# Kernel tuning notes

Hardware: AMD Instinct MI355X
Metric: run time of the kernel (lower is better)

Reference implementation:

```python
import jax, jax.numpy as jnp
import numpy as np

NEG_INF = -1e30


def _cc_attention(q, k, v):
    # q,k: [B,H,W,c], v: [B,H,W,C]
    B, H, W, _ = q.shape
    # vertical scores over column: [B,H,W,H], diag (h==g) masked out
    sv = jnp.einsum('bhwc,bgwc->bhwg', q, k)
    eye = jnp.eye(H, dtype=bool)[:, None, :]  # [H,1,H]
    sv = jnp.where(eye, NEG_INF, sv)
    # horizontal scores over row: [B,H,W,W]
    sh = jnp.einsum('bhwc,bhuc->bhwu', q, k)
    a = jax.nn.softmax(jnp.concatenate([sv, sh], axis=-1), axis=-1)
    av, ah = a[..., :H], a[..., H:H + W]
    yv = jnp.einsum('bhwg,bgwc->bhwc', av, v)
    yh = jnp.einsum('bhwu,bhuc->bhwc', ah, v)
    return yv + yh


def setup_inputs() -> dict:
    key = jax.random.key(0)
    ks = jax.random.split(key, 7)
    B, H, W, C = 8, 96, 96, 512
    c = C // 8
    s = lambda n: 1.0 / np.sqrt(n)
    return {
        'x': jax.random.normal(ks[0], (B, H, W, C), jnp.float32),
        'Wq': jax.random.normal(ks[1], (C, c), jnp.float32) * s(C),
        'bq': jnp.zeros((c,), jnp.float32),
        'Wk': jax.random.normal(ks[2], (C, c), jnp.float32) * s(C),
        'bk': jnp.zeros((c,), jnp.float32),
        'Wv': jax.random.normal(ks[3], (C, C), jnp.float32) * s(C),
        'bv': jnp.zeros((C,), jnp.float32),
        'gamma': jnp.float32(0.5),
    }


def reference(x, Wq, bq, Wk, bk, Wv, bv, gamma):
    # 1x1 convs == per-pixel matmul
    q = jnp.einsum('bhwc,cd->bhwd', x, Wq) + bq
    k = jnp.einsum('bhwc,cd->bhwd', x, Wk) + bk
    v = jnp.einsum('bhwc,cd->bhwd', x, Wv) + bv
    y = _cc_attention(q, k, v) * gamma
    return y + x
```

## Files before the change

kernel.cpp:

```cpp
#include <hip/hip_runtime.h>
#include <hip/hip_bf16.h>


#define NPIX 73728
#define HH 96
#define WW 96
#define CC 512
#define CQ 64
#define PA 384

typedef __attribute__((ext_vector_type(8))) short bf16x8;
typedef __attribute__((ext_vector_type(4))) float f32x4;

__device__ __forceinline__ void async16(const void* g, void* l) {
    __builtin_amdgcn_global_load_lds(
        (const __attribute__((address_space(1))) unsigned int*)g,
        (__attribute__((address_space(3))) unsigned int*)l,
        16, 0, 0);
}

__device__ __forceinline__ short bf16s(float f) {
    __hip_bfloat16 h = __float2bfloat16(f);
    return *reinterpret_cast<short*>(&h);
}

__global__ __launch_bounds__(256) void conv_x(
    const float* __restrict__ x, short* __restrict__ xb)
{
    size_t i8 = ((size_t)blockIdx.x * 256 + threadIdx.x) * 8;
    float4 a = *reinterpret_cast<const float4*>(x + i8);
    float4 b = *reinterpret_cast<const float4*>(x + i8 + 4);
    union { __hip_bfloat16 h[8]; uint4 u; } pk;
    pk.h[0] = __float2bfloat16(a.x); pk.h[1] = __float2bfloat16(a.y);
    pk.h[2] = __float2bfloat16(a.z); pk.h[3] = __float2bfloat16(a.w);
    pk.h[4] = __float2bfloat16(b.x); pk.h[5] = __float2bfloat16(b.y);
    pk.h[6] = __float2bfloat16(b.z); pk.h[7] = __float2bfloat16(b.w);
    *reinterpret_cast<uint4*>(xb + i8) = pk.u;
}

__global__ __launch_bounds__(256) void conv_w(
    const float* __restrict__ W, short* __restrict__ dst, int J)
{
    int idx = blockIdx.x * 256 + threadIdx.x;
    int lane = idx & 63;
    int blk = idx >> 6;
    int ntiles = J >> 4;
    int ntile = blk % ntiles;
    int kb32 = blk / ntiles;
    int krow = kb32 * 32 + (lane >> 4) * 8;
    int col = ntile * 16 + (lane & 15);
    union { __hip_bfloat16 h[8]; uint4 u; } pk;
    #pragma unroll
    for (int j = 0; j < 8; ++j)
        pk.h[j] = __float2bfloat16(W[(size_t)(krow + j) * J + col]);
    *reinterpret_cast<uint4*>(dst + (size_t)idx * 8) = pk.u;
}

template <int BN>
__global__ __launch_bounds__(256) void mfma_proj(
    const short* __restrict__ Xb,
    const short* __restrict__ Wf,
    const float* __restrict__ bias,
    short* __restrict__ out,
    int J)
{
    __shared__ __align__(16) short Albuf[128 * 32];
    const int tid = threadIdx.x;
    const int lane = tid & 63;
    const int w = tid >> 6;
    const int mBase = blockIdx.x * 128;
    const int nBase = blockIdx.y * BN;

    constexpr int MT = (BN == 128) ? 4 : 2;
    constexpr int NT = 4;
    const int wr = (BN == 128) ? (w >> 1) : w;
    const int wc = (BN == 128) ? (w & 1) : 0;
    const int tbase = wr * MT;
    const int nTile0 = (nBase >> 4) + wc * 4;
    const int ntilesJ = J >> 4;

    f32x4 acc[MT][NT];
    #pragma unroll
    for (int i = 0; i < MT; ++i)
        #pragma unroll
        for (int j = 0; j < NT; ++j) {
            f32x4 z = {0.f, 0.f, 0.f, 0.f};
            acc[i][j] = z;
        }

    const int arow0 = lane & 15;
    const int acol0 = (lane >> 4) * 8;

    for (int kb = 0; kb < 16; ++kb) {
        #pragma unroll
        for (int s = 0; s < 2; ++s) {
            int t = w * 2 + s;
            const short* g = Xb + (size_t)(mBase + t * 16 + arow0) * 512 + kb * 32 + acol0;
            async16(g, &Albuf[t * 512]);
        }
        __syncthreads();

        bf16x8 bf[NT];
        #pragma unroll
        for (int jn = 0; jn < NT; ++jn)
            bf[jn] = *reinterpret_cast<const bf16x8*>(
                Wf + ((size_t)(kb * ntilesJ + nTile0 + jn) * 64 + lane) * 8);
        bf16x8 af[MT];
        #pragma unroll
        for (int i = 0; i < MT; ++i)
            af[i] = *reinterpret_cast<const bf16x8*>(&Albuf[(tbase + i) * 512 + lane * 8]);
        #pragma unroll
        for (int i = 0; i < MT; ++i)
            #pragma unroll
            for (int jn = 0; jn < NT; ++jn)
                acc[i][jn] = __builtin_amdgcn_mfma_f32_16x16x32_bf16(
                    af[i], bf[jn], acc[i][jn], 0, 0, 0);
        __syncthreads();
    }

    const int lrow = (lane >> 4) * 4, lcol = lane & 15;
    #pragma unroll
    for (int jn = 0; jn < NT; ++jn) {
        int col = nBase + wc * 64 + jn * 16 + lcol;
        float bc = bias[col];
        #pragma unroll
        for (int i = 0; i < MT; ++i) {
            int row = mBase + wr * (MT * 16) + i * 16 + lrow;
            #pragma unroll
            for (int r = 0; r < 4; ++r) {
                out[(size_t)(row + r) * J + col] = bf16s(acc[i][jn][r] + bc);
            }
        }
    }
}

__global__ __launch_bounds__(256) void proj_v_th(
    const short* __restrict__ Xb,
    const short* __restrict__ Wf,
    const float* __restrict__ bias,
    short* __restrict__ vth)
{
    __shared__ __align__(16) short Albuf[128 * 32];
    const int tid = threadIdx.x;
    const int lane = tid & 63;
    const int w = tid >> 6;
    const int bid = blockIdx.x;
    const int mBase = (bid >> 2) * 128;
    const int nBase = (bid & 3) * 128;

    const int wr = w >> 1, wc = w & 1;
    const int nTile0 = (nBase >> 4) + wc * 4;

    f32x4 acc[4][4];
    #pragma unroll
    for (int i = 0; i < 4; ++i)
        #pragma unroll
        for (int j = 0; j < 4; ++j) {
            f32x4 z = {0.f, 0.f, 0.f, 0.f};
            acc[i][j] = z;
        }

    const int arow0 = lane & 15;
    const int acol0 = (lane >> 4) * 8;

    for (int kb = 0; kb < 16; ++kb) {
        #pragma unroll
        for (int s = 0; s < 2; ++s) {
            int t = w * 2 + s;
            const short* g = Xb + (size_t)(mBase + t * 16 + arow0) * 512 + kb * 32 + acol0;
            async16(g, &Albuf[t * 512]);
        }
        __syncthreads();

        bf16x8 bf[4];
        #pragma unroll
        for (int jn = 0; jn < 4; ++jn)
            bf[jn] = *reinterpret_cast<const bf16x8*>(
                Wf + ((size_t)(kb * 32 + nTile0 + jn) * 64 + lane) * 8);
        bf16x8 af[4];
        #pragma unroll
        for (int i = 0; i < 4; ++i)
            af[i] = *reinterpret_cast<const bf16x8*>(&Albuf[(wr * 4 + i) * 512 + lane * 8]);
        #pragma unroll
        for (int i = 0; i < 4; ++i)
            #pragma unroll
            for (int jn = 0; jn < 4; ++jn)
                acc[i][jn] = __builtin_amdgcn_mfma_f32_16x16x32_bf16(
                    af[i], bf[jn], acc[i][jn], 0, 0, 0);
        __syncthreads();
    }

    const int lrow = (lane >> 4) * 4, lcol = lane & 15;
    #pragma unroll
    for (int jn = 0; jn < 4; ++jn) {
        int col = nBase + wc * 64 + jn * 16 + lcol;
        float bc = bias[col];
        #pragma unroll
        for (int i = 0; i < 4; ++i) {
            int row = mBase + wr * 64 + i * 16 + lrow;
            short4 st;
            st.x = bf16s(acc[i][jn][0] + bc);
            st.y = bf16s(acc[i][jn][1] + bc);
            st.z = bf16s(acc[i][jn][2] + bc);
            st.w = bf16s(acc[i][jn][3] + bc);
            *reinterpret_cast<short4*>(vth + (size_t)col * NPIX + row) = st;
        }
    }
}

__global__ __launch_bounds__(256) void proj_v_tv(
    const short* __restrict__ Xb,
    const short* __restrict__ Wf,
    const float* __restrict__ bias,
    short* __restrict__ vtv)
{
    __shared__ __align__(16) short Albuf[96 * 32];
    const int tid = threadIdx.x;
    const int lane = tid & 63;
    const int wv = tid >> 6;
    const int bid = blockIdx.x;
    const int pair = bid >> 2;
    const int nBase = (bid & 3) * 128;
    const int b = pair / 96;
    const int w = pair - b * 96;
    const size_t colPix = (size_t)b * 9216 + w;
    const size_t wBase = (size_t)b * 9216 + (size_t)w * 96;

    const int wr = wv >> 1, wc = wv & 1;
    const int nTile0 = (nBase >> 4) + wc * 4;

    f32x4 acc[3][4];
    #pragma unroll
    for (int i = 0; i < 3; ++i)
        #pragma unroll
        for (int j = 0; j < 4; ++j) {
            f32x4 z = {0.f, 0.f, 0.f, 0.f};
            acc[i][j] = z;
        }

    const int arow0 = lane & 15;
    const int acol0 = (lane >> 4) * 8;

    for (int kb = 0; kb < 16; ++kb) {
        #pragma unroll
        for (int s = 0; s < 2; ++s) {
            int t = s * 4 + wv;
            if (t < 6) {
                const short* g = Xb + (colPix + (size_t)(t * 16 + arow0) * 96) * 512
                                    + kb * 32 + acol0;
                async16(g, &Albuf[t * 512]);
            }
        }
        __syncthreads();

        bf16x8 bf[4];
        #pragma unroll
        for (int jn = 0; jn < 4; ++jn)
            bf[jn] = *reinterpret_cast<const bf16x8*>(
                Wf + ((size_t)(kb * 32 + nTile0 + jn) * 64 + lane) * 8);
        bf16x8 af[3];
        #pragma unroll
        for (int i = 0; i < 3; ++i)
            af[i] = *reinterpret_cast<const bf16x8*>(&Albuf[(wr * 3 + i) * 512 + lane * 8]);
        #pragma unroll
        for (int i = 0; i < 3; ++i)
            #pragma unroll
            for (int jn = 0; jn < 4; ++jn)
                acc[i][jn] = __builtin_amdgcn_mfma_f32_16x16x32_bf16(
                    af[i], bf[jn], acc[i][jn], 0, 0, 0);
        __syncthreads();
    }

    const int lrow = (lane >> 4) * 4, lcol = lane & 15;
    #pragma unroll
    for (int jn = 0; jn < 4; ++jn) {
        int col = nBase + wc * 64 + jn * 16 + lcol;
        float bc = bias[col];
        #pragma unroll
        for (int i = 0; i < 3; ++i) {
            int h = wr * 48 + i * 16 + lrow;
            short4 st;
            st.x = bf16s(acc[i][jn][0] + bc);
            st.y = bf16s(acc[i][jn][1] + bc);
            st.z = bf16s(acc[i][jn][2] + bc);
            st.w = bf16s(acc[i][jn][3] + bc);
            *reinterpret_cast<short4*>(vtv + (size_t)col * NPIX + wBase + h) = st;
        }
    }
}

__global__ __launch_bounds__(256) void cc_scores(
    const short* __restrict__ Q,
    const short* __restrict__ K,
    float* __restrict__ S)
{
    const int tid = threadIdx.x;
    const int lane = tid & 63;
    const int wv = tid >> 6;
    const int wr = wv >> 1, wc = wv & 1;
    const bool vert = (blockIdx.y == 0);
    const int b = blockIdx.x / 96;
    const int line = blockIdx.x % 96;

    size_t base;
    int rowStride;
    if (vert) { base = (size_t)b * 9216 + line;       rowStride = 96; }
    else      { base = ((size_t)b * 96 + line) * 96;  rowStride = 1;  }

    const int cl = lane & 15;
    const int q8 = (lane >> 4) * 8;

    f32x4 acc[3][3];
    #pragma unroll
    for (int i = 0; i < 3; ++i)
        #pragma unroll
        for (int j = 0; j < 3; ++j) {
            f32x4 z = {0.f, 0.f, 0.f, 0.f};
            acc[i][j] = z;
        }

    #pragma unroll
    for (int kb = 0; kb < 2; ++kb) {
        bf16x8 af[3], bf[3];
        #pragma unroll
        for (int mt = 0; mt < 3; ++mt) {
            size_t n = base + (size_t)(wr * 48 + mt * 16 + cl) * rowStride;
            af[mt] = *reinterpret_cast<const bf16x8*>(Q + n * 64 + kb * 32 + q8);
        }
        #pragma unroll
        for (int nt = 0; nt < 3; ++nt) {
            size_t n = base + (size_t)(wc * 48 + nt * 16 + cl) * rowStride;
            bf[nt] = *reinterpret_cast<const bf16x8*>(K + n * 64 + kb * 32 + q8);
        }
        #pragma unroll
        for (int mt = 0; mt < 3; ++mt)
            #pragma unroll
            for (int nt = 0; nt < 3; ++nt)
                acc[mt][nt] = __builtin_amdgcn_mfma_f32_16x16x32_bf16(
                    af[mt], bf[nt], acc[mt][nt], 0, 0, 0);
    }

    const int lrow = (lane >> 4) * 4;
    const int dirOff = vert ? 0 : 96;
    #pragma unroll
    for (int mt = 0; mt < 3; ++mt) {
        #pragma unroll
        for (int r = 0; r < 4; ++r) {
            int i = wr * 48 + mt * 16 + lrow + r;
            size_t n = base + (size_t)i * rowStride;
            float* srow = S + n * 192 + dirOff;
            #pragma unroll
            for (int nt = 0; nt < 3; ++nt) {
                int j = wc * 48 + nt * 16 + cl;
                srow[j] = (vert && i == j) ? -1e30f : acc[mt][nt][r];
            }
        }
    }
}

__global__ __launch_bounds__(256) void cc_softmax(float* __restrict__ S)
{
    const int tid = threadIdx.x;
    const int lane = tid & 63;
    const size_t n = (size_t)blockIdx.x * 4 + (tid >> 6);
    float* row = S + n * 192;
    float s0 = row[lane], s1 = row[lane + 64], s2 = row[lane + 128];
    float m = fmaxf(s0, fmaxf(s1, s2));
    #pragma unroll
    for (int off = 32; off >= 1; off >>= 1) m = fmaxf(m, __shfl_xor(m, off, 64));
    float e0 = expf(s0 - m), e1 = expf(s1 - m), e2 = expf(s2 - m);
    float sum = e0 + e1 + e2;
    #pragma unroll
    for (int off = 32; off >= 1; off >>= 1) sum += __shfl_xor(sum, off, 64);
    float inv = 1.0f / sum;
    short p0 = bf16s(e0 * inv);
    short p1 = bf16s(e1 * inv);
    short p2 = bf16s(e2 * inv);
    short* av = reinterpret_cast<short*>(row);
    short* ah = av + 96;
    av[lane] = p0;
    if (lane < 32) av[64 + lane] = p1;
    else           ah[lane - 32] = p1;
    ah[32 + lane] = p2;
}

__global__ __launch_bounds__(256) void cc_aggr_v(
    const short* __restrict__ A,
    const short* __restrict__ vtv,
    short* __restrict__ Yv)
{
    const int tid = threadIdx.x;
    const int lane = tid & 63;
    const int wv = tid >> 6;
    const int bid = blockIdx.x;
    const int pair = bid >> 2;
    const int cBase = (bid & 3) * 128;
    const int b = pair / 96;
    const int w = pair - b * 96;
    const size_t pixBase = (size_t)b * 9216 + w;
    const size_t wBase = (size_t)b * 9216 + (size_t)w * 96;

    const int wr = wv >> 1, wc = wv & 1;
    const int cl = lane & 15, q = lane >> 4;

    f32x4 acc[3][4];
    #pragma unroll
    for (int i = 0; i < 3; ++i)
        #pragma unroll
        for (int j = 0; j < 4; ++j) {
            f32x4 z = {0.f, 0.f, 0.f, 0.f};
            acc[i][j] = z;
        }

    #pragma unroll
    for (int kb = 0; kb < 3; ++kb) {
        bf16x8 af[3];
        #pragma unroll
        for (int mt = 0; mt < 3; ++mt) {
            size_t n = pixBase + (size_t)(wr * 48 + mt * 16 + cl) * 96;
            af[mt] = *reinterpret_cast<const bf16x8*>(A + n * PA + kb * 32 + q * 8);
        }
        #pragma unroll
        for (int nt = 0; nt < 4; ++nt) {
            int col = cBase + wc * 64 + nt * 16 + cl;
            bf16x8 bv = *reinterpret_cast<const bf16x8*>(
                vtv + (size_t)col * NPIX + wBase + kb * 32 + q * 8);
            #pragma unroll
            for (int mt = 0; mt < 3; ++mt)
                acc[mt][nt] = __builtin_amdgcn_mfma_f32_16x16x32_bf16(
                    af[mt], bv, acc[mt][nt], 0, 0, 0);
        }
    }

    const int lrow = q * 4;
    #pragma unroll
    for (int mt = 0; mt < 3; ++mt) {
        #pragma unroll
        for (int r = 0; r < 4; ++r) {
            size_t n = pixBase + (size_t)(wr * 48 + mt * 16 + lrow + r) * 96;
            #pragma unroll
            for (int nt = 0; nt < 4; ++nt) {
                int c = cBase + wc * 64 + nt * 16 + cl;
                Yv[n * 512 + c] = bf16s(acc[mt][nt][r]);
            }
        }
    }
}

__global__ __launch_bounds__(256) void cc_aggr_h_final(
    const short* __restrict__ A,
    const short* __restrict__ vth,
    const __hip_bfloat16* __restrict__ Yv,
    const float* __restrict__ X,
    const float* __restrict__ gamma_p,
    float* __restrict__ out)
{
    const int tid = threadIdx.x;
    const int lane = tid & 63;
    const int wv = tid >> 6;
    const int bid = blockIdx.x;
    const int pair = bid >> 2;
    const int cBase = (bid & 3) * 128;
    const size_t rowBase = (size_t)pair * 96;

    const int wr = wv >> 1, wc = wv & 1;
    const int cl = lane & 15, q = lane >> 4;

    f32x4 acc[3][4];
    #pragma unroll
    for (int i = 0; i < 3; ++i)
        #pragma unroll
        for (int j = 0; j < 4; ++j) {
            f32x4 z = {0.f, 0.f, 0.f, 0.f};
            acc[i][j] = z;
        }

    #pragma unroll
    for (int kb = 0; kb < 3; ++kb) {
        bf16x8 af[3];
        #pragma unroll
        for (int mt = 0; mt < 3; ++mt) {
            size_t n = rowBase + (size_t)(wr * 48 + mt * 16 + cl);
            af[mt] = *reinterpret_cast<const bf16x8*>(A + n * PA + 96 + kb * 32 + q * 8);
        }
        #pragma unroll
        for (int nt = 0; nt < 4; ++nt) {
            int col = cBase + wc * 64 + nt * 16 + cl;
            bf16x8 bv = *reinterpret_cast<const bf16x8*>(
                vth + (size_t)col * NPIX + rowBase + kb * 32 + q * 8);
            #pragma unroll
            for (int mt = 0; mt < 3; ++mt)
                acc[mt][nt] = __builtin_amdgcn_mfma_f32_16x16x32_bf16(
                    af[mt], bv, acc[mt][nt], 0, 0, 0);
        }
    }

    const float gm = gamma_p[0];
    const int lrow = q * 4;
    #pragma unroll
    for (int mt = 0; mt < 3; ++mt) {
        #pragma unroll
        for (int r = 0; r < 4; ++r) {
            size_t rowOff = (rowBase + (size_t)(wr * 48 + mt * 16 + lrow + r)) * 512;
            #pragma unroll
            for (int nt = 0; nt < 4; ++nt) {
                size_t off = rowOff + cBase + wc * 64 + nt * 16 + cl;
                out[off] = (acc[mt][nt][r] + __bfloat162float(Yv[off])) * gm + X[off];
            }
        }
    }
}

extern "C" void kernel_launch(void* const* d_in, const int* in_sizes, int n_in,
                              void* d_out, int out_size, void* d_ws, size_t ws_size,
                              hipStream_t stream) {
    const float* x     = (const float*)d_in[0];
    const float* Wq    = (const float*)d_in[1];
    const float* bq    = (const float*)d_in[2];
    const float* Wk    = (const float*)d_in[3];
    const float* bk    = (const float*)d_in[4];
    const float* Wv    = (const float*)d_in[5];
    const float* bv    = (const float*)d_in[6];
    const float* gamma = (const float*)d_in[7];
    float* out = (float*)d_out;

    short* xb  = (short*)d_ws;
    short* Wqf = xb + (size_t)NPIX * 512;
    short* Wkf = Wqf + 512 * 64;
    short* Wvf = Wkf + 512 * 64;
    short* q   = Wvf + 512 * 512;
    short* k   = q + (size_t)NPIX * CQ;
    short* vth = k + (size_t)NPIX * CQ;
    short* vtv = vth + (size_t)NPIX * CC;
    float* S   = (float*)(vtv + (size_t)NPIX * CC);
    short* yv  = xb;

    conv_x<<<NPIX * 512 / 8 / 256, 256, 0, stream>>>(x, xb);
    conv_w<<<16, 256, 0, stream>>>(Wq, Wqf, 64);
    conv_w<<<16, 256, 0, stream>>>(Wk, Wkf, 64);
    conv_w<<<128, 256, 0, stream>>>(Wv, Wvf, 512);

    mfma_proj<64><<<dim3(NPIX / 128, 1), 256, 0, stream>>>(xb, Wqf, bq, q, CQ);
    mfma_proj<64><<<dim3(NPIX / 128, 1), 256, 0, stream>>>(xb, Wkf, bk, k, CQ);
    proj_v_th<<<(NPIX / 128) * 4, 256, 0, stream>>>(xb, Wvf, bv, vth);
    proj_v_tv<<<768 * 4, 256, 0, stream>>>(xb, Wvf, bv, vtv);

    cc_scores<<<dim3(8 * 96, 2), 256, 0, stream>>>(q, k, S);
    cc_softmax<<<NPIX / 4, 256, 0, stream>>>(S);

    cc_aggr_v<<<768 * 4, 256, 0, stream>>>((const short*)S, vtv, yv);
    cc_aggr_h_final<<<768 * 4, 256, 0, stream>>>(
        (const short*)S, vth, (const __hip_bfloat16*)yv, x, gamma, out);
}
```

Baseline: 660.4 us.

## Fuse input bf16 conversion into projections, merge Q/K, transpose V, stage stores via LDS

Removes the separate x-to-bf16 conversion pass by converting fp32 x inline inside the projection kernels. Q and K projections are merged into a single kernel, and the second V projection is replaced by an LDS transpose of the first V output. Score, aggregation and final epilogue stores are staged through LDS so global writes become vectorized and coalesced. The final kernel reads x and Yv with vector loads. This trades extra shared memory and syncs for less redundant GEMM work and memory traffic.

```diff
diff --git a/kernel.cpp b/kernel.cpp
--- a/kernel.cpp
+++ b/kernel.cpp
@@ -3,8 +3,6 @@
 
 
 #define NPIX 73728
-#define HH 96
-#define WW 96
 #define CC 512
 #define CQ 64
 #define PA 384
@@ -12,30 +10,13 @@
 typedef __attribute__((ext_vector_type(8))) short bf16x8;
 typedef __attribute__((ext_vector_type(4))) float f32x4;
 
-__device__ __forceinline__ void async16(const void* g, void* l) {
-    __builtin_amdgcn_global_load_lds(
-        (const __attribute__((address_space(1))) unsigned int*)g,
-        (__attribute__((address_space(3))) unsigned int*)l,
-        16, 0, 0);
-}
-
 __device__ __forceinline__ short bf16s(float f) {
     __hip_bfloat16 h = __float2bfloat16(f);
     return *reinterpret_cast<short*>(&h);
 }
 
-__global__ __launch_bounds__(256) void conv_x(
-    const float* __restrict__ x, short* __restrict__ xb)
-{
-    size_t i8 = ((size_t)blockIdx.x * 256 + threadIdx.x) * 8;
-    float4 a = *reinterpret_cast<const float4*>(x + i8);
-    float4 b = *reinterpret_cast<const float4*>(x + i8 + 4);
-    union { __hip_bfloat16 h[8]; uint4 u; } pk;
-    pk.h[0] = __float2bfloat16(a.x); pk.h[1] = __float2bfloat16(a.y);
-    pk.h[2] = __float2bfloat16(a.z); pk.h[3] = __float2bfloat16(a.w);
-    pk.h[4] = __float2bfloat16(b.x); pk.h[5] = __float2bfloat16(b.y);
-    pk.h[6] = __float2bfloat16(b.z); pk.h[7] = __float2bfloat16(b.w);
-    *reinterpret_cast<uint4*>(xb + i8) = pk.u;
+__device__ __forceinline__ float bf2f(short s) {
+    return __uint_as_float(((unsigned int)(unsigned short)s) << 16);
 }
 
 __global__ __launch_bounds__(256) void conv_w(
@@ -49,96 +30,102 @@
     int kb32 = blk / ntiles;
     int krow = kb32 * 32 + (lane >> 4) * 8;
     int col = ntile * 16 + (lane & 15);
-    union { __hip_bfloat16 h[8]; uint4 u; } pk;
+    union { short h[8]; uint4 u; } pk;
     #pragma unroll
     for (int j = 0; j < 8; ++j)
-        pk.h[j] = __float2bfloat16(W[(size_t)(krow + j) * J + col]);
+        pk.h[j] = bf16s(W[(size_t)(krow + j) * J + col]);
     *reinterpret_cast<uint4*>(dst + (size_t)idx * 8) = pk.u;
 }
 
-template <int BN>
-__global__ __launch_bounds__(256) void mfma_proj(
-    const short* __restrict__ Xb,
-    const short* __restrict__ Wf,
-    const float* __restrict__ bias,
-    short* __restrict__ out,
-    int J)
-{
-    __shared__ __align__(16) short Albuf[128 * 32];
+__global__ __launch_bounds__(256) void proj_qk(
+    const float* __restrict__ x,
+    const short* __restrict__ Wqf, const short* __restrict__ Wkf,
+    const float* __restrict__ bq, const float* __restrict__ bk,
+    short* __restrict__ q, short* __restrict__ k)
+{
+    __shared__ __align__(16) short Sbuf[128 * 136];
     const int tid = threadIdx.x;
     const int lane = tid & 63;
     const int w = tid >> 6;
     const int mBase = blockIdx.x * 128;
-    const int nBase = blockIdx.y * BN;
-
-    constexpr int MT = (BN == 128) ? 4 : 2;
-    constexpr int NT = 4;
-    const int wr = (BN == 128) ? (w >> 1) : w;
-    const int wc = (BN == 128) ? (w & 1) : 0;
-    const int tbase = wr * MT;
-    const int nTile0 = (nBase >> 4) + wc * 4;
-    const int ntilesJ = J >> 4;
-
-    f32x4 acc[MT][NT];
-    #pragma unroll
-    for (int i = 0; i < MT; ++i)
-        #pragma unroll
-        for (int j = 0; j < NT; ++j) {
+    const int wr = w >> 1;
+    const int wsel = w & 1;
+    const short* Wf = wsel ? Wkf : Wqf;
+    const float* bias = wsel ? bk : bq;
+
+    f32x4 acc[4][4];
+    #pragma unroll
+    for (int i = 0; i < 4; ++i)
+        #pragma unroll
+        for (int j = 0; j < 4; ++j) {
             f32x4 z = {0.f, 0.f, 0.f, 0.f};
             acc[i][j] = z;
         }
 
-    const int arow0 = lane & 15;
-    const int acol0 = (lane >> 4) * 8;
-
     for (int kb = 0; kb < 16; ++kb) {
         #pragma unroll
         for (int s = 0; s < 2; ++s) {
-            int t = w * 2 + s;
-            const short* g = Xb + (size_t)(mBase + t * 16 + arow0) * 512 + kb * 32 + acol0;
-            async16(g, &Albuf[t * 512]);
+            int seg = tid + 256 * s;
+            int r = seg >> 2, kq = seg & 3;
+            const float* src = x + (size_t)(mBase + r) * 512 + kb * 32 + kq * 8;
+            float4 f0 = *reinterpret_cast<const float4*>(src);
+            float4 f1 = *reinterpret_cast<const float4*>(src + 4);
+            union { short h[8]; bf16x8 v; } pk;
+            pk.h[0] = bf16s(f0.x); pk.h[1] = bf16s(f0.y);
+            pk.h[2] = bf16s(f0.z); pk.h[3] = bf16s(f0.w);
+            pk.h[4] = bf16s(f1.x); pk.h[5] = bf16s(f1.y);
+            pk.h[6] = bf16s(f1.z); pk.h[7] = bf16s(f1.w);
+            int dlane = (r & 15) + 16 * kq;
+            *reinterpret_cast<bf16x8*>(&Sbuf[(r >> 4) * 512 + dlane * 8]) = pk.v;
         }
         __syncthreads();
 
-        bf16x8 bf[NT];
-        #pragma unroll
-        for (int jn = 0; jn < NT; ++jn)
+        bf16x8 bf[4], af[4];
+        #pragma unroll
+        for (int jn = 0; jn < 4; ++jn)
             bf[jn] = *reinterpret_cast<const bf16x8*>(
-                Wf + ((size_t)(kb * ntilesJ + nTile0 + jn) * 64 + lane) * 8);
-        bf16x8 af[MT];
-        #pragma unroll
-        for (int i = 0; i < MT; ++i)
-            af[i] = *reinterpret_cast<const bf16x8*>(&Albuf[(tbase + i) * 512 + lane * 8]);
-        #pragma unroll
-        for (int i = 0; i < MT; ++i)
-            #pragma unroll
-            for (int jn = 0; jn < NT; ++jn)
+                Wf + ((size_t)(kb * 4 + jn) * 64 + lane) * 8);
+        #pragma unroll
+        for (int i = 0; i < 4; ++i)
+            af[i] = *reinterpret_cast<const bf16x8*>(&Sbuf[(wr * 4 + i) * 512 + lane * 8]);
+        #pragma unroll
+        for (int i = 0; i < 4; ++i)
+            #pragma unroll
+            for (int jn = 0; jn < 4; ++jn)
                 acc[i][jn] = __builtin_amdgcn_mfma_f32_16x16x32_bf16(
                     af[i], bf[jn], acc[i][jn], 0, 0, 0);
         __syncthreads();
     }
 
-    const int lrow = (lane >> 4) * 4, lcol = lane & 15;
-    #pragma unroll
-    for (int jn = 0; jn < NT; ++jn) {
-        int col = nBase + wc * 64 + jn * 16 + lcol;
-        float bc = bias[col];
-        #pragma unroll
-        for (int i = 0; i < MT; ++i) {
-            int row = mBase + wr * (MT * 16) + i * 16 + lrow;
-            #pragma unroll
-            for (int r = 0; r < 4; ++r) {
-                out[(size_t)(row + r) * J + col] = bf16s(acc[i][jn][r] + bc);
-            }
-        }
-    }
-}
-
-__global__ __launch_bounds__(256) void proj_v_th(
-    const short* __restrict__ Xb,
-    const short* __restrict__ Wf,
-    const float* __restrict__ bias,
-    short* __restrict__ vth)
+    const int lrow = (lane >> 4) * 4, cl = lane & 15;
+    #pragma unroll
+    for (int jn = 0; jn < 4; ++jn) {
+        float bc = bias[jn * 16 + cl];
+        #pragma unroll
+        for (int i = 0; i < 4; ++i) {
+            int row = wr * 64 + i * 16 + lrow;
+            #pragma unroll
+            for (int r = 0; r < 4; ++r)
+                Sbuf[(row + r) * 136 + wsel * 64 + jn * 16 + cl] =
+                    bf16s(acc[i][jn][r] + bc);
+        }
+    }
+    __syncthreads();
+    #pragma unroll
+    for (int i = 0; i < 8; ++i) {
+        int id = tid + 256 * i;
+        int arr = id >> 10;
+        int rem = id & 1023;
+        int pix = rem >> 3, cc = rem & 7;
+        bf16x8 vv = *reinterpret_cast<const bf16x8*>(&Sbuf[pix * 136 + arr * 64 + cc * 8]);
+        short* dst = arr ? k : q;
+        *reinterpret_cast<bf16x8*>(dst + (size_t)(mBase + pix) * 64 + cc * 8) = vv;
+    }
+}
+
+__global__ __launch_bounds__(256) void proj_v(
+    const float* __restrict__ x, const short* __restrict__ Wvf,
+    const float* __restrict__ bv, short* __restrict__ vth)
 {
     __shared__ __align__(16) short Albuf[128 * 32];
     const int tid = threadIdx.x;
@@ -160,24 +147,29 @@
             acc[i][j] = z;
         }
 
-    const int arow0 = lane & 15;
-    const int acol0 = (lane >> 4) * 8;
-
     for (int kb = 0; kb < 16; ++kb) {
         #pragma unroll
         for (int s = 0; s < 2; ++s) {
-            int t = w * 2 + s;
-            const short* g = Xb + (size_t)(mBase + t * 16 + arow0) * 512 + kb * 32 + acol0;
-            async16(g, &Albuf[t * 512]);
+            int seg = tid + 256 * s;
+            int r = seg >> 2, kq = seg & 3;
+            const float* src = x + (size_t)(mBase + r) * 512 + kb * 32 + kq * 8;
+            float4 f0 = *reinterpret_cast<const float4*>(src);
+            float4 f1 = *reinterpret_cast<const float4*>(src + 4);
+            union { short h[8]; bf16x8 v; } pk;
+            pk.h[0] = bf16s(f0.x); pk.h[1] = bf16s(f0.y);
+            pk.h[2] = bf16s(f0.z); pk.h[3] = bf16s(f0.w);
+            pk.h[4] = bf16s(f1.x); pk.h[5] = bf16s(f1.y);
+            pk.h[6] = bf16s(f1.z); pk.h[7] = bf16s(f1.w);
+            int dlane = (r & 15) + 16 * kq;
+            *reinterpret_cast<bf16x8*>(&Albuf[(r >> 4) * 512 + dlane * 8]) = pk.v;
         }
         __syncthreads();
 
-        bf16x8 bf[4];
+        bf16x8 bf[4], af[4];
         #pragma unroll
         for (int jn = 0; jn < 4; ++jn)
             bf[jn] = *reinterpret_cast<const bf16x8*>(
-                Wf + ((size_t)(kb * 32 + nTile0 + jn) * 64 + lane) * 8);
-        bf16x8 af[4];
+                Wvf + ((size_t)(kb * 32 + nTile0 + jn) * 64 + lane) * 8);
         #pragma unroll
         for (int i = 0; i < 4; ++i)
             af[i] = *reinterpret_cast<const bf16x8*>(&Albuf[(wr * 4 + i) * 512 + lane * 8]);
@@ -194,7 +186,7 @@
     #pragma unroll
     for (int jn = 0; jn < 4; ++jn) {
         int col = nBase + wc * 64 + jn * 16 + lcol;
-        float bc = bias[col];
+        float bc = bv[col];
         #pragma unroll
         for (int i = 0; i < 4; ++i) {
             int row = mBase + wr * 64 + i * 16 + lrow;
@@ -208,84 +200,28 @@
     }
 }
 
-__global__ __launch_bounds__(256) void proj_v_tv(
-    const short* __restrict__ Xb,
-    const short* __restrict__ Wf,
-    const float* __restrict__ bias,
-    short* __restrict__ vtv)
-{
-    __shared__ __align__(16) short Albuf[96 * 32];
-    const int tid = threadIdx.x;
-    const int lane = tid & 63;
-    const int wv = tid >> 6;
-    const int bid = blockIdx.x;
-    const int pair = bid >> 2;
-    const int nBase = (bid & 3) * 128;
-    const int b = pair / 96;
-    const int w = pair - b * 96;
-    const size_t colPix = (size_t)b * 9216 + w;
-    const size_t wBase = (size_t)b * 9216 + (size_t)w * 96;
-
-    const int wr = wv >> 1, wc = wv & 1;
-    const int nTile0 = (nBase >> 4) + wc * 4;
-
-    f32x4 acc[3][4];
-    #pragma unroll
-    for (int i = 0; i < 3; ++i)
-        #pragma unroll
-        for (int j = 0; j < 4; ++j) {
-            f32x4 z = {0.f, 0.f, 0.f, 0.f};
-            acc[i][j] = z;
-        }
-
-    const int arow0 = lane & 15;
-    const int acol0 = (lane >> 4) * 8;
-
-    for (int kb = 0; kb < 16; ++kb) {
-        #pragma unroll
-        for (int s = 0; s < 2; ++s) {
-            int t = s * 4 + wv;
-            if (t < 6) {
-                const short* g = Xb + (colPix + (size_t)(t * 16 + arow0) * 96) * 512
-                                    + kb * 32 + acol0;
-                async16(g, &Albuf[t * 512]);
-            }
-        }
-        __syncthreads();
-
-        bf16x8 bf[4];
-        #pragma unroll
-        for (int jn = 0; jn < 4; ++jn)
-            bf[jn] = *reinterpret_cast<const bf16x8*>(
-                Wf + ((size_t)(kb * 32 + nTile0 + jn) * 64 + lane) * 8);
-        bf16x8 af[3];
-        #pragma unroll
-        for (int i = 0; i < 3; ++i)
-            af[i] = *reinterpret_cast<const bf16x8*>(&Albuf[(wr * 3 + i) * 512 + lane * 8]);
-        #pragma unroll
-        for (int i = 0; i < 3; ++i)
-            #pragma unroll
-            for (int jn = 0; jn < 4; ++jn)
-                acc[i][jn] = __builtin_amdgcn_mfma_f32_16x16x32_bf16(
-                    af[i], bf[jn], acc[i][jn], 0, 0, 0);
-        __syncthreads();
-    }
-
-    const int lrow = (lane >> 4) * 4, lcol = lane & 15;
-    #pragma unroll
-    for (int jn = 0; jn < 4; ++jn) {
-        int col = nBase + wc * 64 + jn * 16 + lcol;
-        float bc = bias[col];
-        #pragma unroll
-        for (int i = 0; i < 3; ++i) {
-            int h = wr * 48 + i * 16 + lrow;
-            short4 st;
-            st.x = bf16s(acc[i][jn][0] + bc);
-            st.y = bf16s(acc[i][jn][1] + bc);
-            st.z = bf16s(acc[i][jn][2] + bc);
-            st.w = bf16s(acc[i][jn][3] + bc);
-            *reinterpret_cast<short4*>(vtv + (size_t)col * NPIX + wBase + h) = st;
-        }
+__global__ __launch_bounds__(256) void transpose_vtv(
+    const short* __restrict__ vth, short* __restrict__ vtv)
+{
+    __shared__ short T[96 * 97];
+    const int tid = threadIdx.x;
+    const size_t plane = (size_t)blockIdx.x * 9216;
+    const short* src = vth + plane;
+    short* dst = vtv + plane;
+
+    for (int id = tid; id < 1152; id += 256) {
+        int h = id / 12, w8 = (id % 12) * 8;
+        bf16x8 v = *reinterpret_cast<const bf16x8*>(src + h * 96 + w8);
+        #pragma unroll
+        for (int j = 0; j < 8; ++j) T[h * 97 + w8 + j] = v[j];
+    }
+    __syncthreads();
+    for (int id = tid; id < 1152; id += 256) {
+        int ww = id / 12, h8 = (id % 12) * 8;
+        union { short h[8]; bf16x8 v; } pk;
+        #pragma unroll
+        for (int j = 0; j < 8; ++j) pk.h[j] = T[(h8 + j) * 97 + ww];
+        *reinterpret_cast<bf16x8*>(dst + ww * 96 + h8) = pk.v;
     }
 }
 
@@ -294,6 +230,7 @@
     const short* __restrict__ K,
     float* __restrict__ S)
 {
+    __shared__ __align__(16) float Ss[96 * 100];
     const int tid = threadIdx.x;
     const int lane = tid & 63;
     const int wv = tid >> 6;
@@ -341,20 +278,28 @@
     }
 
     const int lrow = (lane >> 4) * 4;
-    const int dirOff = vert ? 0 : 96;
     #pragma unroll
     for (int mt = 0; mt < 3; ++mt) {
         #pragma unroll
         for (int r = 0; r < 4; ++r) {
             int i = wr * 48 + mt * 16 + lrow + r;
-            size_t n = base + (size_t)i * rowStride;
-            float* srow = S + n * 192 + dirOff;
             #pragma unroll
             for (int nt = 0; nt < 3; ++nt) {
                 int j = wc * 48 + nt * 16 + cl;
-                srow[j] = (vert && i == j) ? -1e30f : acc[mt][nt][r];
+                Ss[i * 100 + j] = (vert && i == j) ? -1e30f : acc[mt][nt][r];
             }
         }
+    }
+    __syncthreads();
+
+    const int dirOff = vert ? 0 : 96;
+    #pragma unroll
+    for (int t = 0; t < 9; ++t) {
+        int id = tid + 256 * t;
+        int i = id / 24, j4 = (id % 24) * 4;
+        f32x4 v = *reinterpret_cast<const f32x4*>(&Ss[i * 100 + j4]);
+        size_t n = base + (size_t)i * rowStride;
+        *reinterpret_cast<f32x4*>(S + n * 192 + dirOff + j4) = v;
     }
 }
 
@@ -389,6 +334,7 @@
     const short* __restrict__ vtv,
     short* __restrict__ Yv)
 {
+    __shared__ __align__(16) short Yb[96 * 136];
     const int tid = threadIdx.x;
     const int lane = tid & 63;
     const int wv = tid >> 6;
@@ -437,24 +383,32 @@
     for (int mt = 0; mt < 3; ++mt) {
         #pragma unroll
         for (int r = 0; r < 4; ++r) {
-            size_t n = pixBase + (size_t)(wr * 48 + mt * 16 + lrow + r) * 96;
-            #pragma unroll
-            for (int nt = 0; nt < 4; ++nt) {
-                int c = cBase + wc * 64 + nt * 16 + cl;
-                Yv[n * 512 + c] = bf16s(acc[mt][nt][r]);
-            }
-        }
+            int hl = wr * 48 + mt * 16 + lrow + r;
+            #pragma unroll
+            for (int nt = 0; nt < 4; ++nt)
+                Yb[hl * 136 + wc * 64 + nt * 16 + cl] = bf16s(acc[mt][nt][r]);
+        }
+    }
+    __syncthreads();
+    #pragma unroll
+    for (int i = 0; i < 6; ++i) {
+        int id = tid + 256 * i;
+        int hh = id >> 4, cc = id & 15;
+        bf16x8 v = *reinterpret_cast<const bf16x8*>(&Yb[hh * 136 + cc * 8]);
+        *reinterpret_cast<bf16x8*>(
+            Yv + (pixBase + (size_t)hh * 96) * 512 + cBase + cc * 8) = v;
     }
 }
 
 __global__ __launch_bounds__(256) void cc_aggr_h_final(
     const short* __restrict__ A,
     const short* __restrict__ vth,
-    const __hip_bfloat16* __restrict__ Yv,
+    const short* __restrict__ Yv,
     const float* __restrict__ X,
     const float* __restrict__ gamma_p,
     float* __restrict__ out)
 {
+    __shared__ __align__(16) float Yh[96 * 132];
     const int tid = threadIdx.x;
     const int lane = tid & 63;
     const int wv = tid >> 6;
@@ -495,19 +449,34 @@
         }
     }
 
+    const int lrow = q * 4;
+    #pragma unroll
+    for (int mt = 0; mt < 3; ++mt) {
+        #pragma unroll
+        for (int r = 0; r < 4; ++r) {
+            int wl = wr * 48 + mt * 16 + lrow + r;
+            #pragma unroll
+            for (int nt = 0; nt < 4; ++nt)
+                Yh[wl * 132 + wc * 64 + nt * 16 + cl] = acc[mt][nt][r];
+        }
+    }
+    __syncthreads();
+
     const float gm = gamma_p[0];
-    const int lrow = q * 4;
-    #pragma unroll
-    for (int mt = 0; mt < 3; ++mt) {
-        #pragma unroll
-        for (int r = 0; r < 4; ++r) {
-            size_t rowOff = (rowBase + (size_t)(wr * 48 + mt * 16 + lrow + r)) * 512;
-            #pragma unroll
-            for (int nt = 0; nt < 4; ++nt) {
-                size_t off = rowOff + cBase + wc * 64 + nt * 16 + cl;
-                out[off] = (acc[mt][nt][r] + __bfloat162float(Yv[off])) * gm + X[off];
-            }
-        }
+    #pragma unroll
+    for (int i = 0; i < 12; ++i) {
+        int id = tid + 256 * i;
+        int rw = id >> 5, c4 = (id & 31) * 4;
+        f32x4 yh = *reinterpret_cast<const f32x4*>(&Yh[rw * 132 + c4]);
+        size_t off = (rowBase + rw) * 512 + cBase + c4;
+        float4 xx = *reinterpret_cast<const float4*>(X + off);
+        short4 yv = *reinterpret_cast<const short4*>(Yv + off);
+        float4 o;
+        o.x = (yh[0] + bf2f(yv.x)) * gm + xx.x;
+        o.y = (yh[1] + bf2f(yv.y)) * gm + xx.y;
+        o.z = (yh[2] + bf2f(yv.z)) * gm + xx.z;
+        o.w = (yh[3] + bf2f(yv.w)) * gm + xx.w;
+        *reinterpret_cast<float4*>(out + off) = o;
     }
 }
 
@@ -524,31 +493,28 @@
     const float* gamma = (const float*)d_in[7];
     float* out = (float*)d_out;
 
-    short* xb  = (short*)d_ws;
-    short* Wqf = xb + (size_t)NPIX * 512;
+    short* Wqf = (short*)d_ws;
     short* Wkf = Wqf + 512 * 64;
     short* Wvf = Wkf + 512 * 64;
     short* q   = Wvf + 512 * 512;
     short* k   = q + (size_t)NPIX * CQ;
     short* vth = k + (size_t)NPIX * CQ;
     short* vtv = vth + (size_t)NPIX * CC;
-    float* S   = (float*)(vtv + (size_t)NPIX * CC);
-    short* yv  = xb;
-
-    conv_x<<<NPIX * 512 / 8 / 256, 256, 0, stream>>>(x, xb);
+    short* Yv  = vtv + (size_t)NPIX * CC;
+    float* S   = (float*)(Yv + (size_t)NPIX * CC);
+
     conv_w<<<16, 256, 0, stream>>>(Wq, Wqf, 64);
     conv_w<<<16, 256, 0, stream>>>(Wk, Wkf, 64);
     conv_w<<<128, 256, 0, stream>>>(Wv, Wvf, 512);
 
-    mfma_proj<64><<<dim3(NPIX / 128, 1), 256, 0, stream>>>(xb, Wqf, bq, q, CQ);
-    mfma_proj<64><<<dim3(NPIX / 128, 1), 256, 0, stream>>>(xb, Wkf, bk, k, CQ);
-    proj_v_th<<<(NPIX / 128) * 4, 256, 0, stream>>>(xb, Wvf, bv, vth);
-    proj_v_tv<<<768 * 4, 256, 0, stream>>>(xb, Wvf, bv, vtv);
+    proj_qk<<<NPIX / 128, 256, 0, stream>>>(x, Wqf, Wkf, bq, bk, q, k);
+    proj_v<<<(NPIX / 128) * 4, 256, 0, stream>>>(x, Wvf, bv, vth);
+    transpose_vtv<<<4096, 256, 0, stream>>>(vth, vtv);
 
     cc_scores<<<dim3(8 * 96, 2), 256, 0, stream>>>(q, k, S);
     cc_softmax<<<NPIX / 4, 256, 0, stream>>>(S);
 
-    cc_aggr_v<<<768 * 4, 256, 0, stream>>>((const short*)S, vtv, yv);
+    cc_aggr_v<<<768 * 4, 256, 0, stream>>>((const short*)S, vtv, Yv);
     cc_aggr_h_final<<<768 * 4, 256, 0, stream>>>(
-        (const short*)S, vth, (const __hip_bfloat16*)yv, x, gamma, out);
-}
+        (const short*)S, vth, Yv, x, gamma, out);
+}
```

New measurement: 582.1 us. -11.9%, faster.
